# Performance work log

Measured on AMD Instinct MI355X. Metric: run time of the kernel, lower is better.

## Reference

```python
import jax, jax.numpy as jnp
import numpy as np

N = 50000
E = 800000
IN_DIM = 128
HIDDEN = 128
OUT_DIM = 64
NUM_GRAPHS = 64


def setup_inputs() -> dict:
    key = jax.random.key(0)
    ks = jax.random.split(key, 16)
    x = jax.random.normal(ks[0], (N, IN_DIM), dtype=jnp.float32)
    edge_index = jax.random.randint(ks[1], (2, E), 0, N, dtype=jnp.int32)
    batch = jnp.sort(jax.random.randint(ks[2], (N,), 0, NUM_GRAPHS, dtype=jnp.int32))

    def glorot(k, shape):
        fan_in = shape[1]
        return jax.random.normal(k, shape, dtype=jnp.float32) / jnp.sqrt(jnp.float32(fan_in))

    # SAGEConv params: lin_l (on aggregated neighbors, with bias), lin_r (on self, no bias)
    return {
        "x": x,
        "edge_index": edge_index,
        "batch": batch,
        "W1l": glorot(ks[3], (HIDDEN, IN_DIM)), "b1l": jnp.zeros((HIDDEN,), jnp.float32),
        "W1r": glorot(ks[4], (HIDDEN, IN_DIM)),
        "W2l": glorot(ks[5], (HIDDEN, HIDDEN)), "b2l": jnp.zeros((HIDDEN,), jnp.float32),
        "W2r": glorot(ks[6], (HIDDEN, HIDDEN)),
        "W3l": glorot(ks[7], (HIDDEN, HIDDEN)), "b3l": jnp.zeros((HIDDEN,), jnp.float32),
        "W3r": glorot(ks[8], (HIDDEN, HIDDEN)),
        "Wlin": glorot(ks[9], (OUT_DIM, HIDDEN)), "blin": jnp.zeros((OUT_DIM,), jnp.float32),
    }


def sage_conv(x, src, dst, Wl, bl, Wr):
    # aggr='add': scatter-add source features onto target nodes, then two linears.
    agg = jax.ops.segment_sum(x[src], dst, num_segments=N)  # [N, d_in]
    return agg @ Wl.T + bl + x @ Wr.T


def reference(x, edge_index, batch, W1l, b1l, W1r, W2l, b2l, W2r, W3l, b3l, W3r, Wlin, blin):
    src, dst = edge_index[0], edge_index[1]
    h = jax.nn.relu(sage_conv(x, src, dst, W1l, b1l, W1r))
    # dropout p=0.3 is identity at inference
    h = jax.nn.relu(sage_conv(h, src, dst, W2l, b2l, W2r))
    h = sage_conv(h, src, dst, W3l, b3l, W3r)
    # global mean pool over graphs
    sums = jax.ops.segment_sum(h, batch, num_segments=NUM_GRAPHS)  # [G, hidden]
    counts = jax.ops.segment_sum(jnp.ones((N,), h.dtype), batch, num_segments=NUM_GRAPHS)
    pooled = sums / jnp.maximum(counts, 1.0)[:, None]
    return pooled @ Wlin.T + blin  # [G, out_dim]
```

## Files before the change

### kernel.cpp

```cpp
#include <hip/hip_runtime.h>


typedef __bf16 bf16x8 __attribute__((ext_vector_type(8)));
typedef float f32x4 __attribute__((ext_vector_type(4)));
typedef float f32x2 __attribute__((ext_vector_type(2)));

#define BINB 160
#define NBMAX 512

static __device__ __forceinline__ float bf2f(unsigned short u) {
    union { unsigned u; float f; } c; c.u = (unsigned)u << 16; return c.f;
}
static __device__ __forceinline__ unsigned short f2bf(float f) {
    unsigned u = __builtin_bit_cast(unsigned, f);
    return (unsigned short)((u + 0x7fffu + ((u >> 16) & 1u)) >> 16);
}
static __device__ __forceinline__ uint2 pk8_fp8(const float* f) {
    int lo = 0, hi = 0;
    lo = __builtin_amdgcn_cvt_pk_fp8_f32(f[0], f[1], lo, false);
    lo = __builtin_amdgcn_cvt_pk_fp8_f32(f[2], f[3], lo, true);
    hi = __builtin_amdgcn_cvt_pk_fp8_f32(f[4], f[5], hi, false);
    hi = __builtin_amdgcn_cvt_pk_fp8_f32(f[6], f[7], hi, true);
    return make_uint2((unsigned)lo, (unsigned)hi);
}
static __device__ __forceinline__ unsigned char f2fp8(float v) {
    return (unsigned char)(__builtin_amdgcn_cvt_pk_fp8_f32(v, v, 0, false) & 0xff);
}

__global__ __launch_bounds__(256) void k_bincast(
    const int* __restrict__ dst, int* __restrict__ cnt_mat, int E, int nb, int epb,
    const float* __restrict__ x, unsigned short* __restrict__ xb,
    unsigned char* __restrict__ x8, int n8, int nxblk,
    const float* __restrict__ W1l, const float* __restrict__ W1r,
    const float* __restrict__ W2l, const float* __restrict__ W2r,
    unsigned short* __restrict__ Whi)
{
    __shared__ int lc[NBMAX];
    int bid = blockIdx.x;
    if (bid < BINB) {
        for (int i = threadIdx.x; i < nb; i += 256) lc[i] = 0;
        __syncthreads();
        int b0 = bid * epb;
        int b1 = min(b0 + epb, E);
        for (int i = b0 + threadIdx.x; i < b1; i += 256)
            atomicAdd(&lc[dst[i] >> 7], 1);
        __syncthreads();
        for (int i = threadIdx.x; i < nb; i += 256)
            cnt_mat[i * BINB + bid] = lc[i];
    } else if (bid < BINB + nxblk) {
        int i = (bid - BINB) * 256 + threadIdx.x;
        if (i >= n8) return;
        float f[8];
        *(float4*)(f + 0) = *(const float4*)(x + (size_t)i * 8);
        *(float4*)(f + 4) = *(const float4*)(x + (size_t)i * 8 + 4);
        ushort4 oa, ob;
        oa.x = f2bf(f[0]); oa.y = f2bf(f[1]); oa.z = f2bf(f[2]); oa.w = f2bf(f[3]);
        ob.x = f2bf(f[4]); ob.y = f2bf(f[5]); ob.z = f2bf(f[6]); ob.w = f2bf(f[7]);
        int node = i >> 4, c = i & 15;
        size_t dstb = (size_t)(node >> 4) * 2048 + (size_t)(c >> 2) * 512
                    + (size_t)((c & 3) * 16 + (node & 15)) * 8;
        *(ushort4*)(xb + dstb) = oa;
        *(ushort4*)(xb + dstb + 4) = ob;
        *(uint2*)(x8 + (size_t)i * 8) = pk8_fp8(f);
    } else {
        int wb = bid - BINB - nxblk;
        int layer = wb >> 7;
        int j = wb & 127;
        int k = threadIdx.x;
        const float* Wl = (layer == 0) ? W1l : W2l;
        const float* Wr = (layer == 0) ? W1r : W2r;
        float w = (k < 128) ? Wl[j * 128 + k] : Wr[j * 128 + k - 128];
        int js = j >> 4, mr = j & 15;
        int s = k >> 5, quad = (k >> 3) & 3, e = k & 7;
        size_t o = (size_t)layer * 32768
                 + ((size_t)(js * 8 + s) * 64 + quad * 16 + mr) * 8 + e;
        Whi[o] = f2bf(w);
    }
}

__global__ __launch_bounds__(256) void k_mrowscan(
    const int* __restrict__ cnt_mat, int* __restrict__ rowloc, int* __restrict__ btot)
{
    __shared__ int s[256];
    int b = blockIdx.x;
    int t = threadIdx.x;
    int v = (t < BINB) ? cnt_mat[b * BINB + t] : 0;
    s[t] = v;
    __syncthreads();
#pragma unroll
    for (int off = 1; off < 256; off <<= 1) {
        int u = (t >= off) ? s[t - off] : 0;
        __syncthreads();
        s[t] += u;
        __syncthreads();
    }
    if (t < BINB) rowloc[b * BINB + t] = s[t] - v;
    if (t == 255) btot[b] = s[255];
}

__global__ __launch_bounds__(256) void k_scan2b(
    const int* __restrict__ btot, int* __restrict__ bbase, int nb, int* __restrict__ total_out)
{
    __shared__ int s[256];
    int t = threadIdx.x;
    int per = (nb + 255) / 256;
    int s0 = t * per, e0 = min(s0 + per, nb);
    int sum = 0;
    for (int i = s0; i < e0; ++i) sum += btot[i];
    s[t] = sum;
    __syncthreads();
#pragma unroll
    for (int off = 1; off < 256; off <<= 1) {
        int u = (t >= off) ? s[t - off] : 0;
        __syncthreads();
        s[t] += u;
        __syncthreads();
    }
    int run = s[t] - sum;
    for (int i = s0; i < e0; ++i) { bbase[i] = run; run += btot[i]; }
    if (t == 255) *total_out = s[255];
}

__global__ __launch_bounds__(256) void k_binscatter(
    const int* __restrict__ ei, const int* __restrict__ rowloc, const int* __restrict__ bbase,
    unsigned* __restrict__ binned, int E, int nb, int epb)
{
    __shared__ int lofs[NBMAX];
    __shared__ int lcnt[NBMAX];
    for (int i = threadIdx.x; i < nb; i += 256) {
        lofs[i] = rowloc[i * BINB + blockIdx.x] + bbase[i];
        lcnt[i] = 0;
    }
    __syncthreads();
    int b0 = blockIdx.x * epb;
    int b1 = min(b0 + epb, E);
    for (int i = b0 + threadIdx.x; i < b1; i += 256) {
        int s = ei[i];
        int d = ei[E + i];
        int b = d >> 7;
        int r = atomicAdd(&lcnt[b], 1);
        binned[lofs[b] + r] = (unsigned)s | ((unsigned)(d & 127) << 16);
    }
}

__global__ __launch_bounds__(256) void k_fillfine2(
    const unsigned* __restrict__ binned, const int* __restrict__ bbase,
    const int* __restrict__ batch, int* __restrict__ starts,
    unsigned short* __restrict__ csr_src, int* __restrict__ gestart,
    int E, int nb, int n)
{
    __shared__ int lc[128];
    __shared__ int lpos[128];
    int b = blockIdx.x;
    int t = threadIdx.x;
    int node0 = b << 7;
    int bs = bbase[b];
    int be = (b == nb - 1) ? E : bbase[b + 1];
    if (t < 128) lc[t] = 0;
    __syncthreads();
    for (int i = bs + t; i < be; i += 256)
        atomicAdd(&lc[(binned[i] >> 16) & 127], 1);
    __syncthreads();
    int v = (t < 128) ? lc[t] : 0;
    if (t < 128) lpos[t] = v;
    __syncthreads();
#pragma unroll
    for (int off = 1; off < 128; off <<= 1) {
        int u = (t >= off && t < 128) ? lpos[t - off] : 0;
        __syncthreads();
        if (t < 128) lpos[t] += u;
        __syncthreads();
    }
    int excl = (t < 128) ? (lpos[t] - v) : 0;
    __syncthreads();
    if (t < 128) {
        int node = node0 + t;
        if (node < n) {
            int st = bs + excl;
            starts[node] = st;
            int bc = batch[node];
            int bp = (node == 0) ? -1 : batch[node - 1];
            for (int g = bp + 1; g <= bc; ++g) gestart[g] = st;
            if (node == n - 1)
                for (int g = bc + 1; g <= 64; ++g) gestart[g] = E;
        }
        lpos[t] = bs + excl;
    }
    if (b == nb - 1 && t == 0) starts[n] = E;
    __syncthreads();
    for (int i = bs + t; i < be; i += 256) {
        unsigned e = binned[i];
        int slot = atomicAdd(&lpos[(e >> 16) & 127], 1);
        csr_src[slot] = (unsigned short)(e & 0xffffu);
    }
}

#define ACC8(v)                                                         \
    do {                                                                \
        f32x2 p0 = __builtin_amdgcn_cvt_pk_f32_fp8((v).x, false);       \
        f32x2 p1 = __builtin_amdgcn_cvt_pk_f32_fp8((v).x, true);        \
        f32x2 p2 = __builtin_amdgcn_cvt_pk_f32_fp8((v).y, false);       \
        f32x2 p3 = __builtin_amdgcn_cvt_pk_f32_fp8((v).y, true);        \
        a0 += p0.x; a1 += p0.y; a2 += p1.x; a3 += p1.y;                 \
        a4 += p2.x; a5 += p2.y; a6 += p3.x; a7 += p3.y;                 \
    } while (0)

#define ACC_SEG(sbeg, send)                                             \
    for (int base = (sbeg); base < (send); base += 64) {                \
        int cnt = min(64, (send) - base);                               \
        int idx = (base + lane < (send)) ? (int)csr[base + lane] : 0;   \
        int j = 0;                                                      \
        for (; j + 16 <= cnt; j += 16) {                                \
            int s0 = __shfl(idx, j + eg);                               \
            int s1 = __shfl(idx, j + 4 + eg);                           \
            int s2 = __shfl(idx, j + 8 + eg);                           \
            int s3 = __shfl(idx, j + 12 + eg);                          \
            uint2 v0 = *(const uint2*)(hrow + (size_t)s0 * 128);        \
            uint2 v1 = *(const uint2*)(hrow + (size_t)s1 * 128);        \
            uint2 v2 = *(const uint2*)(hrow + (size_t)s2 * 128);        \
            uint2 v3 = *(const uint2*)(hrow + (size_t)s3 * 128);        \
            ACC8(v0);                                                   \
            ACC8(v1);                                                   \
            ACC8(v2);                                                   \
            ACC8(v3);                                                   \
        }                                                               \
        for (; j + 8 <= cnt; j += 8) {                                  \
            int s0 = __shfl(idx, j + eg);                               \
            int s1 = __shfl(idx, j + 4 + eg);                           \
            uint2 v0 = *(const uint2*)(hrow + (size_t)s0 * 128);        \
            uint2 v1 = *(const uint2*)(hrow + (size_t)s1 * 128);        \
            ACC8(v0);                                                   \
            ACC8(v1);                                                   \
        }                                                               \
        for (; j + 4 <= cnt; j += 4) {                                  \
            int s0 = __shfl(idx, j + eg);                               \
            uint2 v0 = *(const uint2*)(hrow + (size_t)s0 * 128);        \
            ACC8(v0);                                                   \
        }                                                               \
        if (j < cnt) {                                                  \
            int k = j + eg;                                             \
            int sm = __shfl(idx, (k < cnt) ? k : (cnt - 1));            \
            uint2 v = *(const uint2*)(hrow + (size_t)sm * 128);         \
            if (k >= cnt) v = make_uint2(0u, 0u);                       \
            ACC8(v);                                                    \
        }                                                               \
    }

#define REDUCE8()                                                       \
    a0 += __shfl_xor(a0, 16); a0 += __shfl_xor(a0, 32);                 \
    a1 += __shfl_xor(a1, 16); a1 += __shfl_xor(a1, 32);                 \
    a2 += __shfl_xor(a2, 16); a2 += __shfl_xor(a2, 32);                 \
    a3 += __shfl_xor(a3, 16); a3 += __shfl_xor(a3, 32);                 \
    a4 += __shfl_xor(a4, 16); a4 += __shfl_xor(a4, 32);                 \
    a5 += __shfl_xor(a5, 16); a5 += __shfl_xor(a5, 32);                 \
    a6 += __shfl_xor(a6, 16); a6 += __shfl_xor(a6, 32);                 \
    a7 += __shfl_xor(a7, 16); a7 += __shfl_xor(a7, 32);

__global__ __launch_bounds__(512) void k_layer(
    const unsigned char* __restrict__ h8_in, const int* __restrict__ starts,
    const unsigned short* __restrict__ csr, const unsigned short* __restrict__ hf,
    const unsigned short* __restrict__ Whi, const float* __restrict__ bl,
    unsigned short* __restrict__ outf, unsigned char* __restrict__ out8,
    int n, int do_relu, int do_outf)
{
    __shared__ unsigned short sagg[4096];
    int t = threadIdx.x;
    int wv = t >> 6;
    int lane = t & 63;
    int node0 = blockIdx.x * 32;

    {
        int eg = lane >> 4;
        int fb = lane & 15;
        const unsigned char* hrow = h8_in + fb * 8;
        for (int r = 0; r < 4; ++r) {
            int node = node0 + wv * 4 + r;
            if (node >= n) break;
            float a0 = 0.f, a1 = 0.f, a2 = 0.f, a3 = 0.f,
                  a4 = 0.f, a5 = 0.f, a6 = 0.f, a7 = 0.f;
            int s = starts[node], e = starts[node + 1];

            ACC_SEG(s, e)
            REDUCE8()

            if (eg == 0) {
                int ln = node - node0;
                unsigned u0 = (unsigned)f2bf(a0) | ((unsigned)f2bf(a1) << 16);
                unsigned u1 = (unsigned)f2bf(a2) | ((unsigned)f2bf(a3) << 16);
                unsigned u2 = (unsigned)f2bf(a4) | ((unsigned)f2bf(a5) << 16);
                unsigned u3 = (unsigned)f2bf(a6) | ((unsigned)f2bf(a7) << 16);
                size_t dst = (size_t)(ln >> 4) * 2048 + (size_t)(fb >> 2) * 512
                           + (size_t)((fb & 3) * 16 + (ln & 15)) * 8;
                *(uint4*)(sagg + dst) = make_uint4(u0, u1, u2, u3);
            }
        }
    }
    __syncthreads();

    int quad = lane >> 4;
    int mr = lane & 15;
    int js = wv;
    int jbase = js * 16;
    size_t nb0 = (size_t)blockIdx.x * 2;

    f32x4 acc0 = (f32x4){0.f, 0.f, 0.f, 0.f};
    f32x4 acc1 = (f32x4){0.f, 0.f, 0.f, 0.f};

    const unsigned short* wp = Whi + (size_t)js * 4096 + (size_t)lane * 8;
    const unsigned short* sa = sagg + (size_t)lane * 8;
    const unsigned short* ha = hf + nb0 * 2048 + (size_t)lane * 8;

    uint4 pb[2][3];
#define LAYER_LOAD(s, b)                                                  \
    do {                                                                  \
        pb[b][0] = *(const uint4*)(wp + (size_t)(s) * 512);               \
        if ((s) < 4) {                                                    \
            pb[b][1] = *(const uint4*)(sa + (size_t)(s) * 512);           \
            pb[b][2] = *(const uint4*)(sa + (size_t)(s) * 512 + 2048);    \
        } else {                                                          \
            pb[b][1] = *(const uint4*)(ha + (size_t)((s) - 4) * 512);     \
            pb[b][2] = *(const uint4*)(ha + (size_t)((s) - 4) * 512 + 2048); \
        }                                                                 \
    } while (0)

    LAYER_LOAD(0, 0);
    LAYER_LOAD(1, 1);
#pragma unroll
    for (int s = 0; s < 8; ++s) {
        int b = s & 1;
        bf16x8 bh = __builtin_bit_cast(bf16x8, pb[b][0]);
        bf16x8 A0 = __builtin_bit_cast(bf16x8, pb[b][1]);
        bf16x8 A1 = __builtin_bit_cast(bf16x8, pb[b][2]);
        acc0 = __builtin_amdgcn_mfma_f32_16x16x32_bf16(A0, bh, acc0, 0, 0, 0);
        acc1 = __builtin_amdgcn_mfma_f32_16x16x32_bf16(A1, bh, acc1, 0, 0, 0);
        if (s + 2 < 8) LAYER_LOAD(s + 2, b);
    }
#undef LAYER_LOAD

    int col = jbase + mr;
    float bias = bl[col];
    int q2 = (col >> 3) & 3;
    int e2 = col & 7;
    int so = col >> 5;

#pragma unroll
    for (int mi = 0; mi < 2; ++mi) {
        f32x4 a = mi ? acc1 : acc0;
#pragma unroll
        for (int r = 0; r < 4; ++r) {
            int node = node0 + mi * 16 + quad * 4 + r;
            if (node >= n) continue;
            float v = a[r] + bias;
            if (do_relu) v = fmaxf(v, 0.f);
            if (do_outf)
                outf[(size_t)(node >> 4) * 2048 + (size_t)so * 512
                     + (size_t)(q2 * 16 + (node & 15)) * 8 + e2] = f2bf(v);
            out8[(size_t)node * 128 + col] = f2fp8(v);
        }
    }
}

__global__ __launch_bounds__(256) void k_tail(
    const unsigned char* __restrict__ h8, const unsigned short* __restrict__ csr,
    const int* __restrict__ gestart, float* __restrict__ gsumE,
    const int* __restrict__ batch, float* __restrict__ gsumP,
    int E, int n, int apgrid)
{
    __shared__ float gbuf[4][128];
    int t = threadIdx.x;
    if ((int)blockIdx.x >= apgrid) {
        int wave = ((blockIdx.x - apgrid) * 256 + t) >> 6;
        int lane = t & 63;
        int r0 = wave * 16;
        if (r0 >= n) return;
        int r1 = min(r0 + 16, n);
        int cur = batch[r0];
        float ax = 0.f, ay = 0.f;
        for (int i = r0; i < r1; ++i) {
            int g = batch[i];
            uchar2 v = *(const uchar2*)(h8 + (size_t)i * 128 + lane * 2);
            if (g != cur) {
                atomicAdd(&gsumP[cur * 128 + lane * 2], ax);
                atomicAdd(&gsumP[cur * 128 + lane * 2 + 1], ay);
                ax = 0.f; ay = 0.f; cur = g;
            }
            unsigned pk = (unsigned)v.x | ((unsigned)v.y << 8);
            f32x2 p = __builtin_amdgcn_cvt_pk_f32_fp8((int)pk, false);
            ax += p.x;
            ay += p.y;
        }
        atomicAdd(&gsumP[cur * 128 + lane * 2], ax);
        atomicAdd(&gsumP[cur * 128 + lane * 2 + 1], ay);
        return;
    }

    int B0 = blockIdx.x * 256;
    if (B0 >= E) return;
    for (int q = t; q < 512; q += 256) gbuf[q >> 7][q & 127] = 0.f;
    __syncthreads();

    int lo = 0, hi = 63;
    while (lo < hi) { int m = (lo + hi + 1) >> 1; if (gestart[m] <= B0) lo = m; else hi = m - 1; }
    int gblk = lo;

    int wv = t >> 6;
    int lane = t & 63;
    int e0 = B0 + wv * 64;
    if (e0 < E) {
        int e1 = min(e0 + 64, E);
        int eg = lane >> 4;
        int fb = lane & 15;
        const unsigned char* hrow = h8 + fb * 8;

        int g = gblk;
        while (g < 63 && gestart[g + 1] <= e0) ++g;

        float a0 = 0.f, a1 = 0.f, a2 = 0.f, a3 = 0.f,
              a4 = 0.f, a5 = 0.f, a6 = 0.f, a7 = 0.f;
        int cur = e0;
        bool dirty = false;
        while (cur < e1) {
            int gend = gestart[g + 1];
            int send = min(e1, gend);

            ACC_SEG(cur, send)
            dirty = true;
            cur = send;

            if (cur == gend) {
                REDUCE8()
                if (eg == 0) {
                    int gi = g - gblk;
                    if (gi < 4) {
                        float* d = &gbuf[gi][fb * 8];
                        atomicAdd(d + 0, a0); atomicAdd(d + 1, a1);
                        atomicAdd(d + 2, a2); atomicAdd(d + 3, a3);
                        atomicAdd(d + 4, a4); atomicAdd(d + 5, a5);
                        atomicAdd(d + 6, a6); atomicAdd(d + 7, a7);
                    } else {
                        float* d = &gsumE[(size_t)g * 128 + fb * 8];
                        atomicAdd(d + 0, a0); atomicAdd(d + 1, a1);
                        atomicAdd(d + 2, a2); atomicAdd(d + 3, a3);
                        atomicAdd(d + 4, a4); atomicAdd(d + 5, a5);
                        atomicAdd(d + 6, a6); atomicAdd(d + 7, a7);
                    }
                }
                a0 = a1 = a2 = a3 = a4 = a5 = a6 = a7 = 0.f;
                dirty = false;
                ++g;
                while (g < 63 && gestart[g + 1] <= cur) ++g;
            }
        }
        if (dirty) {
            REDUCE8()
            if (eg == 0) {
                int gi = g - gblk;
                if (gi < 4) {
                    float* d = &gbuf[gi][fb * 8];
                    atomicAdd(d + 0, a0); atomicAdd(d + 1, a1);
                    atomicAdd(d + 2, a2); atomicAdd(d + 3, a3);
                    atomicAdd(d + 4, a4); atomicAdd(d + 5, a5);
                    atomicAdd(d + 6, a6); atomicAdd(d + 7, a7);
                } else {
                    float* d = &gsumE[(size_t)g * 128 + fb * 8];
                    atomicAdd(d + 0, a0); atomicAdd(d + 1, a1);
                    atomicAdd(d + 2, a2); atomicAdd(d + 3, a3);
                    atomicAdd(d + 4, a4); atomicAdd(d + 5, a5);
                    atomicAdd(d + 6, a6); atomicAdd(d + 7, a7);
                }
            }
        }
    }
    __syncthreads();
    for (int q = t; q < 512; q += 256) {
        int sl = q >> 7, c = q & 127;
        float v = gbuf[sl][c];
        if (v != 0.f && gblk + sl < 64)
            atomicAdd(&gsumE[(size_t)(gblk + sl) * 128 + c], v);
    }
}

__global__ __launch_bounds__(128) void k_final(
    const float* __restrict__ gsumE, const float* __restrict__ gsumP,
    const int* __restrict__ batch,
    const float* __restrict__ W3l, const float* __restrict__ b3,
    const float* __restrict__ W3r,
    const float* __restrict__ Wlin, const float* __restrict__ blin,
    float* __restrict__ out, int n)
{
    __shared__ float tmp[128];
    int g = blockIdx.x;
    int t = threadIdx.x;
    int lo = 0, hi = n;
    while (lo < hi) { int m = (lo + hi) >> 1; if (batch[m] < g) lo = m + 1; else hi = m; }
    int lb = lo;
    hi = n;
    while (lo < hi) { int m = (lo + hi) >> 1; if (batch[m] < g + 1) lo = m + 1; else hi = m; }
    int cnt = lo - lb;
    float inv = (cnt > 0) ? 1.f / (float)cnt : 0.f;

    float acc = 0.f;
    for (int k = 0; k < 128; ++k)
        acc += gsumE[g * 128 + k] * W3l[t * 128 + k]
             + gsumP[g * 128 + k] * W3r[t * 128 + k];
    tmp[t] = acc * inv + ((cnt > 0) ? b3[t] : 0.f);
    __syncthreads();

    if (t < 64) {
        float o = 0.f;
        for (int k = 0; k < 128; ++k)
            o += tmp[k] * Wlin[t * 128 + k];
        out[g * 64 + t] = o + blin[t];
    }
}

extern "C" void kernel_launch(void* const* d_in, const int* in_sizes, int n_in,
                              void* d_out, int out_size, void* d_ws, size_t ws_size,
                              hipStream_t stream) {
    const float* x     = (const float*)d_in[0];
    const int*   ei    = (const int*)d_in[1];
    const int*   batch = (const int*)d_in[2];
    const float* W1l = (const float*)d_in[3];
    const float* b1l = (const float*)d_in[4];
    const float* W1r = (const float*)d_in[5];
    const float* W2l = (const float*)d_in[6];
    const float* b2l = (const float*)d_in[7];
    const float* W2r = (const float*)d_in[8];
    const float* W3l = (const float*)d_in[9];
    const float* b3l = (const float*)d_in[10];
    const float* W3r = (const float*)d_in[11];
    const float* Wlin = (const float*)d_in[12];
    const float* blin = (const float*)d_in[13];

    const int N = in_sizes[2];
    const int E = in_sizes[1] / 2;
    const int nb = (N + 127) >> 7;
    const int epb = (E + BINB - 1) / BINB;

    size_t off = 0;
    auto alloc = [&](size_t bytes) {
        void* p = (char*)d_ws + off;
        off += (bytes + 255) & ~(size_t)255;
        return p;
    };
    int* csr_start = (int*)alloc((size_t)(N + 1) * 4);
    int* cnt_mat   = (int*)alloc((size_t)nb * BINB * 4);
    int* rowloc    = (int*)alloc((size_t)nb * BINB * 4);
    int* btot      = (int*)alloc((size_t)NBMAX * 4);
    int* bbase     = (int*)alloc((size_t)NBMAX * 4);
    int* gestart   = (int*)alloc(256 + 64);
    unsigned short* csr_src = (unsigned short*)alloc((size_t)E * 2);
    unsigned*       binned  = (unsigned*)alloc((size_t)E * 4);
    unsigned short* x_bf = (unsigned short*)alloc((size_t)N * 128 * 2 + 65536);
    unsigned short* hA   = (unsigned short*)alloc((size_t)N * 128 * 2 + 65536);
    unsigned char*  x8   = (unsigned char*)alloc((size_t)N * 128);
    unsigned char*  h1_8 = (unsigned char*)alloc((size_t)N * 128);
    unsigned char*  h2_8 = (unsigned char*)alloc((size_t)N * 128);
    unsigned short* Whi = (unsigned short*)alloc(2 * 128 * 256 * 2);
    float* gsumE = (float*)alloc((size_t)64 * 128 * 4);
    float* gsumP = (float*)alloc((size_t)64 * 128 * 4);
    (void)ws_size;

    hipMemsetAsync(gsumE, 0, (size_t)2 * 64 * 128 * 4, stream);

    int n8 = N * 128 / 8;
    int nxblk = (n8 + 255) / 256;
    k_bincast<<<BINB + nxblk + 256, 256, 0, stream>>>(
        ei + E, cnt_mat, E, nb, epb,
        x, x_bf, x8, n8, nxblk, W1l, W1r, W2l, W2r, Whi);
    k_mrowscan<<<nb, 256, 0, stream>>>(cnt_mat, rowloc, btot);
    k_scan2b<<<1, 256, 0, stream>>>(btot, bbase, nb, csr_start + N);
    k_binscatter<<<BINB, 256, 0, stream>>>(ei, rowloc, bbase, binned, E, nb, epb);
    k_fillfine2<<<nb, 256, 0, stream>>>(binned, bbase, batch, csr_start, csr_src,
                                        gestart, E, nb, N);

    int lay_grid = (N + 31) / 32;
    int pool_grid = (((N + 15) / 16) + 3) / 4;
    int aggpool_grid = (E + 255) / 256;

    k_layer<<<lay_grid, 512, 0, stream>>>(x8, csr_start, csr_src, x_bf,
                                          Whi, b1l, hA, h1_8, N, 1, 1);
    k_layer<<<lay_grid, 512, 0, stream>>>(h1_8, csr_start, csr_src, hA,
                                          Whi + 32768, b2l, hA, h2_8, N, 1, 0);
    k_tail<<<aggpool_grid + pool_grid, 256, 0, stream>>>(
        h2_8, csr_src, gestart, gsumE, batch, gsumP, E, N, aggpool_grid);

    k_final<<<64, 128, 0, stream>>>(gsumE, gsumP, batch, W3l, b3l, W3r,
                                    Wlin, blin, (float*)d_out, N);
}
```

Baseline: 244.5 us.

## Replace layer-3 edge aggregation with graph-by-source count matrix MFMA product

Layer-3 aggregation pooled per graph is rewritten as a dense product: a per-(graph, source) edge count histogram is built in the first kernel and multiplied on MFMA units against a transposed fp8 copy of h2 written by layer 2. This replaces the old edge-walking k_tail gather. k_layer is also reshaped to 16 nodes per 256-thread block with each wave covering two output column tiles, prefetching CSR indices for its four nodes, and using packed f32x2 accumulation. The cost is a large 64xN uint32 count matrix that must be zeroed and read, plus atomics in the histogram; counts are cast to bf16 and h2 passes through fp8 then bf16, so precision changes.

```diff
diff --git a/kernel.cpp b/kernel.cpp
--- a/kernel.cpp
+++ b/kernel.cpp
@@ -8,9 +8,6 @@
 #define BINB 160
 #define NBMAX 512
 
-static __device__ __forceinline__ float bf2f(unsigned short u) {
-    union { unsigned u; float f; } c; c.u = (unsigned)u << 16; return c.f;
-}
 static __device__ __forceinline__ unsigned short f2bf(float f) {
     unsigned u = __builtin_bit_cast(unsigned, f);
     return (unsigned short)((u + 0x7fffu + ((u >> 16) & 1u)) >> 16);
@@ -28,12 +25,13 @@
 }
 
 __global__ __launch_bounds__(256) void k_bincast(
-    const int* __restrict__ dst, int* __restrict__ cnt_mat, int E, int nb, int epb,
+    const int* __restrict__ ei, int* __restrict__ cnt_mat, int E, int nb, int epb,
     const float* __restrict__ x, unsigned short* __restrict__ xb,
     unsigned char* __restrict__ x8, int n8, int nxblk,
     const float* __restrict__ W1l, const float* __restrict__ W1r,
     const float* __restrict__ W2l, const float* __restrict__ W2r,
-    unsigned short* __restrict__ Whi)
+    unsigned short* __restrict__ Whi,
+    const int* __restrict__ batch, unsigned* __restrict__ cnt, int nsp, int hepb)
 {
     __shared__ int lc[NBMAX];
     int bid = blockIdx.x;
@@ -43,7 +41,7 @@
         int b0 = bid * epb;
         int b1 = min(b0 + epb, E);
         for (int i = b0 + threadIdx.x; i < b1; i += 256)
-            atomicAdd(&lc[dst[i] >> 7], 1);
+            atomicAdd(&lc[ei[E + i] >> 7], 1);
         __syncthreads();
         for (int i = threadIdx.x; i < nb; i += 256)
             cnt_mat[i * BINB + bid] = lc[i];
@@ -62,7 +60,7 @@
         *(ushort4*)(xb + dstb) = oa;
         *(ushort4*)(xb + dstb + 4) = ob;
         *(uint2*)(x8 + (size_t)i * 8) = pk8_fp8(f);
-    } else {
+    } else if (bid < BINB + nxblk + 256) {
         int wb = bid - BINB - nxblk;
         int layer = wb >> 7;
         int j = wb & 127;
@@ -75,6 +73,16 @@
         size_t o = (size_t)layer * 32768
                  + ((size_t)(js * 8 + s) * 64 + quad * 16 + mr) * 8 + e;
         Whi[o] = f2bf(w);
+    } else {
+        int hb = bid - BINB - nxblk - 256;
+        int b0 = hb * hepb;
+        int b1 = min(b0 + hepb, E);
+        for (int i = b0 + threadIdx.x; i < b1; i += 256) {
+            int s = ei[i];
+            int d = ei[E + i];
+            int g = batch[d];
+            atomicAdd(&cnt[(size_t)g * nsp + s], 1u);
+        }
     }
 }
 
@@ -195,54 +203,43 @@
     }
 }
 
-#define ACC8(v)                                                         \
+#define ACC8P(v)                                                        \
     do {                                                                \
         f32x2 p0 = __builtin_amdgcn_cvt_pk_f32_fp8((v).x, false);       \
         f32x2 p1 = __builtin_amdgcn_cvt_pk_f32_fp8((v).x, true);        \
         f32x2 p2 = __builtin_amdgcn_cvt_pk_f32_fp8((v).y, false);       \
         f32x2 p3 = __builtin_amdgcn_cvt_pk_f32_fp8((v).y, true);        \
-        a0 += p0.x; a1 += p0.y; a2 += p1.x; a3 += p1.y;                 \
-        a4 += p2.x; a5 += p2.y; a6 += p3.x; a7 += p3.y;                 \
+        A01 += p0; A23 += p1; A45 += p2; A67 += p3;                     \
     } while (0)
 
-#define ACC_SEG(sbeg, send)                                             \
-    for (int base = (sbeg); base < (send); base += 64) {                \
-        int cnt = min(64, (send) - base);                               \
-        int idx = (base + lane < (send)) ? (int)csr[base + lane] : 0;   \
+#define PROC_CHUNK(idxv, cntv)                                          \
+    {                                                                   \
         int j = 0;                                                      \
-        for (; j + 16 <= cnt; j += 16) {                                \
-            int s0 = __shfl(idx, j + eg);                               \
-            int s1 = __shfl(idx, j + 4 + eg);                           \
-            int s2 = __shfl(idx, j + 8 + eg);                           \
-            int s3 = __shfl(idx, j + 12 + eg);                          \
+        for (; j + 16 <= (cntv); j += 16) {                             \
+            int s0 = __shfl((int)(idxv), j + eg);                       \
+            int s1 = __shfl((int)(idxv), j + 4 + eg);                   \
+            int s2 = __shfl((int)(idxv), j + 8 + eg);                   \
+            int s3 = __shfl((int)(idxv), j + 12 + eg);                  \
             uint2 v0 = *(const uint2*)(hrow + (size_t)s0 * 128);        \
             uint2 v1 = *(const uint2*)(hrow + (size_t)s1 * 128);        \
             uint2 v2 = *(const uint2*)(hrow + (size_t)s2 * 128);        \
             uint2 v3 = *(const uint2*)(hrow + (size_t)s3 * 128);        \
-            ACC8(v0);                                                   \
-            ACC8(v1);                                                   \
-            ACC8(v2);                                                   \
-            ACC8(v3);                                                   \
+            ACC8P(v0);                                                  \
+            ACC8P(v1);                                                  \
+            ACC8P(v2);                                                  \
+            ACC8P(v3);                                                  \
         }                                                               \
-        for (; j + 8 <= cnt; j += 8) {                                  \
-            int s0 = __shfl(idx, j + eg);                               \
-            int s1 = __shfl(idx, j + 4 + eg);                           \
+        for (; j + 4 <= (cntv); j += 4) {                               \
+            int s0 = __shfl((int)(idxv), j + eg);                       \
             uint2 v0 = *(const uint2*)(hrow + (size_t)s0 * 128);        \
-            uint2 v1 = *(const uint2*)(hrow + (size_t)s1 * 128);        \
-            ACC8(v0);                                                   \
-            ACC8(v1);                                                   \
+            ACC8P(v0);                                                  \
         }                                                               \
-        for (; j + 4 <= cnt; j += 4) {                                  \
-            int s0 = __shfl(idx, j + eg);                               \
-            uint2 v0 = *(const uint2*)(hrow + (size_t)s0 * 128);        \
-            ACC8(v0);                                                   \
-        }                                                               \
-        if (j < cnt) {                                                  \
+        if (j < (cntv)) {                                               \
             int k = j + eg;                                             \
-            int sm = __shfl(idx, (k < cnt) ? k : (cnt - 1));            \
+            int sm = __shfl((int)(idxv), (k < (cntv)) ? k : ((cntv) - 1)); \
             uint2 v = *(const uint2*)(hrow + (size_t)sm * 128);         \
-            if (k >= cnt) v = make_uint2(0u, 0u);                       \
-            ACC8(v);                                                    \
+            if (k >= (cntv)) v = make_uint2(0u, 0u);                    \
+            ACC8P(v);                                                   \
         }                                                               \
     }
 
@@ -256,41 +253,60 @@
     a6 += __shfl_xor(a6, 16); a6 += __shfl_xor(a6, 32);                 \
     a7 += __shfl_xor(a7, 16); a7 += __shfl_xor(a7, 32);
 
-__global__ __launch_bounds__(512) void k_layer(
+__global__ __launch_bounds__(256) void k_layer(
     const unsigned char* __restrict__ h8_in, const int* __restrict__ starts,
     const unsigned short* __restrict__ csr, const unsigned short* __restrict__ hf,
     const unsigned short* __restrict__ Whi, const float* __restrict__ bl,
     unsigned short* __restrict__ outf, unsigned char* __restrict__ out8,
-    int n, int do_relu, int do_outf)
-{
-    __shared__ unsigned short sagg[4096];
+    unsigned char* __restrict__ h2t,
+    int n, int nsp, int do_outf, int do_h2t)
+{
+    __shared__ unsigned short sagg[2048];
     int t = threadIdx.x;
     int wv = t >> 6;
     int lane = t & 63;
-    int node0 = blockIdx.x * 32;
+    int node0 = blockIdx.x * 16;
 
     {
         int eg = lane >> 4;
         int fb = lane & 15;
         const unsigned char* hrow = h8_in + fb * 8;
+        int nodeA = node0 + wv * 4;
+        int st[5];
+#pragma unroll
+        for (int r = 0; r < 5; ++r) {
+            int nn = nodeA + r;
+            st[r] = starts[nn > n ? n : nn];
+        }
+        unsigned idx4[4];
+#pragma unroll
+        for (int r = 0; r < 4; ++r)
+            idx4[r] = (st[r] + lane < st[r + 1]) ? (unsigned)csr[st[r] + lane] : 0u;
+
+#pragma unroll
         for (int r = 0; r < 4; ++r) {
-            int node = node0 + wv * 4 + r;
+            int node = nodeA + r;
             if (node >= n) break;
-            float a0 = 0.f, a1 = 0.f, a2 = 0.f, a3 = 0.f,
-                  a4 = 0.f, a5 = 0.f, a6 = 0.f, a7 = 0.f;
-            int s = starts[node], e = starts[node + 1];
-
-            ACC_SEG(s, e)
+            f32x2 A01 = (f32x2){0.f, 0.f}, A23 = (f32x2){0.f, 0.f},
+                  A45 = (f32x2){0.f, 0.f}, A67 = (f32x2){0.f, 0.f};
+            int deg = st[r + 1] - st[r];
+            int c0 = min(64, deg);
+            PROC_CHUNK(idx4[r], c0)
+            for (int base = st[r] + 64; base < st[r + 1]; base += 64) {
+                int cnt2 = min(64, st[r + 1] - base);
+                unsigned idx = (base + lane < st[r + 1]) ? (unsigned)csr[base + lane] : 0u;
+                PROC_CHUNK(idx, cnt2)
+            }
+            float a0 = A01.x, a1 = A01.y, a2 = A23.x, a3 = A23.y,
+                  a4 = A45.x, a5 = A45.y, a6 = A67.x, a7 = A67.y;
             REDUCE8()
-
             if (eg == 0) {
                 int ln = node - node0;
                 unsigned u0 = (unsigned)f2bf(a0) | ((unsigned)f2bf(a1) << 16);
                 unsigned u1 = (unsigned)f2bf(a2) | ((unsigned)f2bf(a3) << 16);
                 unsigned u2 = (unsigned)f2bf(a4) | ((unsigned)f2bf(a5) << 16);
                 unsigned u3 = (unsigned)f2bf(a6) | ((unsigned)f2bf(a7) << 16);
-                size_t dst = (size_t)(ln >> 4) * 2048 + (size_t)(fb >> 2) * 512
-                           + (size_t)((fb & 3) * 16 + (ln & 15)) * 8;
+                size_t dst = (size_t)(fb >> 2) * 512 + (size_t)((fb & 3) * 16 + ln) * 8;
                 *(uint4*)(sagg + dst) = make_uint4(u0, u1, u2, u3);
             }
         }
@@ -299,28 +315,23 @@
 
     int quad = lane >> 4;
     int mr = lane & 15;
-    int js = wv;
-    int jbase = js * 16;
-    size_t nb0 = (size_t)blockIdx.x * 2;
+    int js0 = wv * 2;
 
     f32x4 acc0 = (f32x4){0.f, 0.f, 0.f, 0.f};
     f32x4 acc1 = (f32x4){0.f, 0.f, 0.f, 0.f};
 
-    const unsigned short* wp = Whi + (size_t)js * 4096 + (size_t)lane * 8;
+    const unsigned short* wp = Whi + (size_t)js0 * 4096 + (size_t)lane * 8;
     const unsigned short* sa = sagg + (size_t)lane * 8;
-    const unsigned short* ha = hf + nb0 * 2048 + (size_t)lane * 8;
+    const unsigned short* ha = hf + (size_t)blockIdx.x * 2048 + (size_t)lane * 8;
 
     uint4 pb[2][3];
 #define LAYER_LOAD(s, b)                                                  \
     do {                                                                  \
         pb[b][0] = *(const uint4*)(wp + (size_t)(s) * 512);               \
-        if ((s) < 4) {                                                    \
-            pb[b][1] = *(const uint4*)(sa + (size_t)(s) * 512);           \
-            pb[b][2] = *(const uint4*)(sa + (size_t)(s) * 512 + 2048);    \
-        } else {                                                          \
-            pb[b][1] = *(const uint4*)(ha + (size_t)((s) - 4) * 512);     \
-            pb[b][2] = *(const uint4*)(ha + (size_t)((s) - 4) * 512 + 2048); \
-        }                                                                 \
+        pb[b][1] = *(const uint4*)(wp + 4096 + (size_t)(s) * 512);        \
+        pb[b][2] = ((s) < 4)                                              \
+            ? *(const uint4*)(sa + (size_t)(s) * 512)                     \
+            : *(const uint4*)(ha + (size_t)((s) - 4) * 512);              \
     } while (0)
 
     LAYER_LOAD(0, 0);
@@ -328,48 +339,54 @@
 #pragma unroll
     for (int s = 0; s < 8; ++s) {
         int b = s & 1;
-        bf16x8 bh = __builtin_bit_cast(bf16x8, pb[b][0]);
-        bf16x8 A0 = __builtin_bit_cast(bf16x8, pb[b][1]);
-        bf16x8 A1 = __builtin_bit_cast(bf16x8, pb[b][2]);
-        acc0 = __builtin_amdgcn_mfma_f32_16x16x32_bf16(A0, bh, acc0, 0, 0, 0);
-        acc1 = __builtin_amdgcn_mfma_f32_16x16x32_bf16(A1, bh, acc1, 0, 0, 0);
+        bf16x8 bh0 = __builtin_bit_cast(bf16x8, pb[b][0]);
+        bf16x8 bh1 = __builtin_bit_cast(bf16x8, pb[b][1]);
+        bf16x8 A0 = __builtin_bit_cast(bf16x8, pb[b][2]);
+        acc0 = __builtin_amdgcn_mfma_f32_16x16x32_bf16(A0, bh0, acc0, 0, 0, 0);
+        acc1 = __builtin_amdgcn_mfma_f32_16x16x32_bf16(A0, bh1, acc1, 0, 0, 0);
         if (s + 2 < 8) LAYER_LOAD(s + 2, b);
     }
 #undef LAYER_LOAD
-
-    int col = jbase + mr;
-    float bias = bl[col];
-    int q2 = (col >> 3) & 3;
-    int e2 = col & 7;
-    int so = col >> 5;
 
 #pragma unroll
     for (int mi = 0; mi < 2; ++mi) {
         f32x4 a = mi ? acc1 : acc0;
+        int col = (js0 + mi) * 16 + mr;
+        float bias = bl[col];
+        int q2 = (col >> 3) & 3;
+        int e2 = col & 7;
+        int so = col >> 5;
+        float vr[4];
 #pragma unroll
         for (int r = 0; r < 4; ++r) {
-            int node = node0 + mi * 16 + quad * 4 + r;
-            if (node >= n) continue;
+            int node = node0 + quad * 4 + r;
             float v = a[r] + bias;
-            if (do_relu) v = fmaxf(v, 0.f);
-            if (do_outf)
-                outf[(size_t)(node >> 4) * 2048 + (size_t)so * 512
-                     + (size_t)(q2 * 16 + (node & 15)) * 8 + e2] = f2bf(v);
-            out8[(size_t)node * 128 + col] = f2fp8(v);
-        }
-    }
-}
-
-__global__ __launch_bounds__(256) void k_tail(
-    const unsigned char* __restrict__ h8, const unsigned short* __restrict__ csr,
-    const int* __restrict__ gestart, float* __restrict__ gsumE,
-    const int* __restrict__ batch, float* __restrict__ gsumP,
-    int E, int n, int apgrid)
-{
-    __shared__ float gbuf[4][128];
+            v = fmaxf(v, 0.f);
+            vr[r] = (node < n) ? v : 0.f;
+            if (node < n) {
+                if (do_outf)
+                    outf[(size_t)(node >> 4) * 2048 + (size_t)so * 512
+                         + (size_t)(q2 * 16 + (node & 15)) * 8 + e2] = f2bf(v);
+                out8[(size_t)node * 128 + col] = f2fp8(v);
+            }
+        }
+        if (do_h2t) {
+            int pk = __builtin_amdgcn_cvt_pk_fp8_f32(vr[0], vr[1], 0, false);
+            pk = __builtin_amdgcn_cvt_pk_fp8_f32(vr[2], vr[3], pk, true);
+            *(unsigned*)(h2t + (size_t)col * nsp + node0 + quad * 4) = (unsigned)pk;
+        }
+    }
+}
+
+__global__ __launch_bounds__(256) void k_gsum(
+    const unsigned* __restrict__ cnt, const unsigned char* __restrict__ h2t,
+    const unsigned char* __restrict__ h8, const int* __restrict__ batch,
+    float* __restrict__ gsumE, float* __restrict__ gsumP,
+    int n, int nsp, int ksteps, int gb)
+{
     int t = threadIdx.x;
-    if ((int)blockIdx.x >= apgrid) {
-        int wave = ((blockIdx.x - apgrid) * 256 + t) >> 6;
+    if ((int)blockIdx.x >= gb) {
+        int wave = ((blockIdx.x - gb) * 256 + t) >> 6;
         int lane = t & 63;
         int r0 = wave * 16;
         if (r0 >= n) return;
@@ -394,89 +411,57 @@
         return;
     }
 
-    int B0 = blockIdx.x * 256;
-    if (B0 >= E) return;
-    for (int q = t; q < 512; q += 256) gbuf[q >> 7][q & 127] = 0.f;
-    __syncthreads();
-
-    int lo = 0, hi = 63;
-    while (lo < hi) { int m = (lo + hi + 1) >> 1; if (gestart[m] <= B0) lo = m; else hi = m - 1; }
-    int gblk = lo;
-
     int wv = t >> 6;
     int lane = t & 63;
-    int e0 = B0 + wv * 64;
-    if (e0 < E) {
-        int e1 = min(e0 + 64, E);
-        int eg = lane >> 4;
-        int fb = lane & 15;
-        const unsigned char* hrow = h8 + fb * 8;
-
-        int g = gblk;
-        while (g < 63 && gestart[g + 1] <= e0) ++g;
-
-        float a0 = 0.f, a1 = 0.f, a2 = 0.f, a3 = 0.f,
-              a4 = 0.f, a5 = 0.f, a6 = 0.f, a7 = 0.f;
-        int cur = e0;
-        bool dirty = false;
-        while (cur < e1) {
-            int gend = gestart[g + 1];
-            int send = min(e1, gend);
-
-            ACC_SEG(cur, send)
-            dirty = true;
-            cur = send;
-
-            if (cur == gend) {
-                REDUCE8()
-                if (eg == 0) {
-                    int gi = g - gblk;
-                    if (gi < 4) {
-                        float* d = &gbuf[gi][fb * 8];
-                        atomicAdd(d + 0, a0); atomicAdd(d + 1, a1);
-                        atomicAdd(d + 2, a2); atomicAdd(d + 3, a3);
-                        atomicAdd(d + 4, a4); atomicAdd(d + 5, a5);
-                        atomicAdd(d + 6, a6); atomicAdd(d + 7, a7);
-                    } else {
-                        float* d = &gsumE[(size_t)g * 128 + fb * 8];
-                        atomicAdd(d + 0, a0); atomicAdd(d + 1, a1);
-                        atomicAdd(d + 2, a2); atomicAdd(d + 3, a3);
-                        atomicAdd(d + 4, a4); atomicAdd(d + 5, a5);
-                        atomicAdd(d + 6, a6); atomicAdd(d + 7, a7);
-                    }
-                }
-                a0 = a1 = a2 = a3 = a4 = a5 = a6 = a7 = 0.f;
-                dirty = false;
-                ++g;
-                while (g < 63 && gestart[g + 1] <= cur) ++g;
-            }
-        }
-        if (dirty) {
-            REDUCE8()
-            if (eg == 0) {
-                int gi = g - gblk;
-                if (gi < 4) {
-                    float* d = &gbuf[gi][fb * 8];
-                    atomicAdd(d + 0, a0); atomicAdd(d + 1, a1);
-                    atomicAdd(d + 2, a2); atomicAdd(d + 3, a3);
-                    atomicAdd(d + 4, a4); atomicAdd(d + 5, a5);
-                    atomicAdd(d + 6, a6); atomicAdd(d + 7, a7);
-                } else {
-                    float* d = &gsumE[(size_t)g * 128 + fb * 8];
-                    atomicAdd(d + 0, a0); atomicAdd(d + 1, a1);
-                    atomicAdd(d + 2, a2); atomicAdd(d + 3, a3);
-                    atomicAdd(d + 4, a4); atomicAdd(d + 5, a5);
-                    atomicAdd(d + 6, a6); atomicAdd(d + 7, a7);
-                }
-            }
-        }
-    }
-    __syncthreads();
-    for (int q = t; q < 512; q += 256) {
-        int sl = q >> 7, c = q & 127;
-        float v = gbuf[sl][c];
-        if (v != 0.f && gblk + sl < 64)
-            atomicAdd(&gsumE[(size_t)(gblk + sl) * 128 + c], v);
+    int fast = lane & 15;
+    int kc = (lane >> 4) * 8;
+    int kpb = (ksteps + gb - 1) / gb;
+    int k0 = blockIdx.x * kpb, k1 = min(k0 + kpb, ksteps);
+    if (k0 >= k1) return;
+
+    f32x4 acc[8];
+#pragma unroll
+    for (int i = 0; i < 8; ++i) acc[i] = (f32x4){0.f, 0.f, 0.f, 0.f};
+
+    const unsigned* ap = cnt + (size_t)(wv * 16 + fast) * nsp + kc;
+    const unsigned char* bp = h2t + (size_t)fast * nsp + kc;
+
+    for (int ks = k0; ks < k1; ++ks) {
+        int kb = ks * 32;
+        uint4 c0 = *(const uint4*)(ap + kb);
+        uint4 c1 = *(const uint4*)(ap + kb + 4);
+        unsigned q0 = (unsigned)f2bf((float)c0.x) | ((unsigned)f2bf((float)c0.y) << 16);
+        unsigned q1 = (unsigned)f2bf((float)c0.z) | ((unsigned)f2bf((float)c0.w) << 16);
+        unsigned q2 = (unsigned)f2bf((float)c1.x) | ((unsigned)f2bf((float)c1.y) << 16);
+        unsigned q3 = (unsigned)f2bf((float)c1.z) | ((unsigned)f2bf((float)c1.w) << 16);
+        uint4 au = make_uint4(q0, q1, q2, q3);
+        bf16x8 af = __builtin_bit_cast(bf16x8, au);
+#pragma unroll
+        for (int ft = 0; ft < 8; ++ft) {
+            uint2 bb = *(const uint2*)(bp + (size_t)ft * 16 * nsp + kb);
+            f32x2 p0 = __builtin_amdgcn_cvt_pk_f32_fp8(bb.x, false);
+            f32x2 p1 = __builtin_amdgcn_cvt_pk_f32_fp8(bb.x, true);
+            f32x2 p2 = __builtin_amdgcn_cvt_pk_f32_fp8(bb.y, false);
+            f32x2 p3 = __builtin_amdgcn_cvt_pk_f32_fp8(bb.y, true);
+            unsigned b0 = (unsigned)f2bf(p0.x) | ((unsigned)f2bf(p0.y) << 16);
+            unsigned b1 = (unsigned)f2bf(p1.x) | ((unsigned)f2bf(p1.y) << 16);
+            unsigned b2 = (unsigned)f2bf(p2.x) | ((unsigned)f2bf(p2.y) << 16);
+            unsigned b3 = (unsigned)f2bf(p3.x) | ((unsigned)f2bf(p3.y) << 16);
+            uint4 bu = make_uint4(b0, b1, b2, b3);
+            bf16x8 bf = __builtin_bit_cast(bf16x8, bu);
+            acc[ft] = __builtin_amdgcn_mfma_f32_16x16x32_bf16(af, bf, acc[ft], 0, 0, 0);
+        }
+    }
+
+    int quad = lane >> 4;
+    int mr = lane & 15;
+    int gg = wv * 16 + quad * 4;
+#pragma unroll
+    for (int ft = 0; ft < 8; ++ft) {
+        int col = ft * 16 + mr;
+#pragma unroll
+        for (int r = 0; r < 4; ++r)
+            atomicAdd(&gsumE[(size_t)(gg + r) * 128 + col], acc[ft][r]);
     }
 }
 
@@ -536,6 +521,8 @@
     const int E = in_sizes[1] / 2;
     const int nb = (N + 127) >> 7;
     const int epb = (E + BINB - 1) / BINB;
+    const int NSP = ((N + 16 + 31) / 32) * 32;
+    const int KSTEPS = NSP / 32;
 
     size_t off = 0;
     auto alloc = [&](size_t bytes) {
@@ -556,34 +543,40 @@
     unsigned char*  x8   = (unsigned char*)alloc((size_t)N * 128);
     unsigned char*  h1_8 = (unsigned char*)alloc((size_t)N * 128);
     unsigned char*  h2_8 = (unsigned char*)alloc((size_t)N * 128);
+    unsigned char*  h2T  = (unsigned char*)alloc((size_t)128 * NSP);
     unsigned short* Whi = (unsigned short*)alloc(2 * 128 * 256 * 2);
+    unsigned* cnt  = (unsigned*)alloc((size_t)64 * NSP * 4);
     float* gsumE = (float*)alloc((size_t)64 * 128 * 4);
     float* gsumP = (float*)alloc((size_t)64 * 128 * 4);
     (void)ws_size;
 
-    hipMemsetAsync(gsumE, 0, (size_t)2 * 64 * 128 * 4, stream);
+    hipMemsetAsync(cnt, 0, (size_t)64 * NSP * 4 + (size_t)2 * 64 * 128 * 4, stream);
 
     int n8 = N * 128 / 8;
     int nxblk = (n8 + 255) / 256;
-    k_bincast<<<BINB + nxblk + 256, 256, 0, stream>>>(
-        ei + E, cnt_mat, E, nb, epb,
-        x, x_bf, x8, n8, nxblk, W1l, W1r, W2l, W2r, Whi);
+    const int HISTB = 256;
+    int hepb = (E + HISTB - 1) / HISTB;
+    k_bincast<<<BINB + nxblk + 256 + HISTB, 256, 0, stream>>>(
+        ei, cnt_mat, E, nb, epb,
+        x, x_bf, x8, n8, nxblk, W1l, W1r, W2l, W2r, Whi,
+        batch, cnt, NSP, hepb);
     k_mrowscan<<<nb, 256, 0, stream>>>(cnt_mat, rowloc, btot);
     k_scan2b<<<1, 256, 0, stream>>>(btot, bbase, nb, csr_start + N);
     k_binscatter<<<BINB, 256, 0, stream>>>(ei, rowloc, bbase, binned, E, nb, epb);
     k_fillfine2<<<nb, 256, 0, stream>>>(binned, bbase, batch, csr_start, csr_src,
                                         gestart, E, nb, N);
 
-    int lay_grid = (N + 31) / 32;
+    int lay_grid  = (N + 15) / 16;
+    int lay2_grid = NSP / 16;
     int pool_grid = (((N + 15) / 16) + 3) / 4;
-    int aggpool_grid = (E + 255) / 256;
-
-    k_layer<<<lay_grid, 512, 0, stream>>>(x8, csr_start, csr_src, x_bf,
-                                          Whi, b1l, hA, h1_8, N, 1, 1);
-    k_layer<<<lay_grid, 512, 0, stream>>>(h1_8, csr_start, csr_src, hA,
-                                          Whi + 32768, b2l, hA, h2_8, N, 1, 0);
-    k_tail<<<aggpool_grid + pool_grid, 256, 0, stream>>>(
-        h2_8, csr_src, gestart, gsumE, batch, gsumP, E, N, aggpool_grid);
+    const int GB = 256;
+
+    k_layer<<<lay_grid, 256, 0, stream>>>(x8, csr_start, csr_src, x_bf,
+                                          Whi, b1l, hA, h1_8, h2T, N, NSP, 1, 0);
+    k_layer<<<lay2_grid, 256, 0, stream>>>(h1_8, csr_start, csr_src, hA,
+                                           Whi + 32768, b2l, hA, h2_8, h2T, N, NSP, 0, 1);
+    k_gsum<<<GB + pool_grid, 256, 0, stream>>>(cnt, h2T, h2_8, batch,
+                                               gsumE, gsumP, N, NSP, KSTEPS, GB);
 
     k_final<<<64, 128, 0, stream>>>(gsumE, gsumP, batch, W3l, b3l, W3r,
                                     Wlin, blin, (float*)d_out, N);
```

Measured after the change: 288.1 us. 17.8% more time.
